# Optimization experiments

Measured on AMD Instinct MI355X. Metric: run time of the kernel, lower is better.

## Reference

```python
import jax, jax.numpy as jnp
import numpy as np

B = 64        # number of graph segments
BASE = 384    # mean verts per segment
LMAX = 512    # pad length (counts in [256, 512])
H_DIM = 256
H_DIV = 128   # h_dim // h_dim_div
HEADS = 4
DH = H_DIV // HEADS  # 32


def _counts(seed):
    rng = np.random.default_rng(seed)
    d = rng.integers(-128, 129, B)
    d[1::2] = -d[::2]            # paired so the total is exactly B*BASE
    return (BASE + d).astype(np.int64)


def _pad_indices(counts, L):
    # Gather indices/mask mapping packed ragged tokens -> padded [B, L].
    counts = np.asarray(counts)
    off = np.concatenate([[0], np.cumsum(counts)[:-1]])
    ar = np.arange(L)[None, :]
    mask = ar < counts[:, None]
    idx = np.where(mask, off[:, None] + ar, 0)
    return idx, mask


def setup_inputs() -> dict:
    key = jax.random.key(0)
    ks = jax.random.split(key, 16)
    src_num_verts = _counts(0)
    dst_num_verts = _counts(1)
    total = B * BASE  # 24576 for both src and dst

    def w(k, shape):
        return 0.02 * jax.random.normal(k, shape, jnp.float32)

    return {
        'src_h': jax.random.normal(ks[0], (total, H_DIM), jnp.float32),
        'dst_h': jax.random.normal(ks[1], (total, H_DIM), jnp.float32),
        'src_num_verts': src_num_verts,
        'dst_num_verts': dst_num_verts,
        # 1x1 Conv1d == linear over channels
        'Wq': w(ks[2], (H_DIV, H_DIM)), 'bq': w(ks[3], (H_DIV,)),
        'Wk': w(ks[4], (H_DIV, H_DIM)), 'bk': w(ks[5], (H_DIV,)),
        'Wv': w(ks[6], (H_DIV, H_DIM)), 'bv': w(ks[7], (H_DIV,)),
        'Wm': w(ks[8], (H_DIV, H_DIV)), 'bm': w(ks[9], (H_DIV,)),
        'W1': w(ks[10], (H_DIM, H_DIM + H_DIV)), 'b1': w(ks[11], (H_DIM,)),
        'g1': 1.0 + 0.1 * jax.random.normal(ks[12], (H_DIM,), jnp.float32),
        'be1': w(ks[13], (H_DIM,)),
        'rm1': w(ks[14], (H_DIM,)),
        'rv1': jax.random.uniform(ks[15], (H_DIM,), jnp.float32, 0.5, 1.5),
        'W2': w(jax.random.fold_in(key, 100), (H_DIM, H_DIM)),
        'b2': w(jax.random.fold_in(key, 101), (H_DIM,)),
        'g2': 1.0 + 0.1 * jax.random.normal(jax.random.fold_in(key, 102), (H_DIM,), jnp.float32),
        'be2': w(jax.random.fold_in(key, 103), (H_DIM,)),
        'rm2': w(jax.random.fold_in(key, 104), (H_DIM,)),
        'rv2': jax.random.uniform(jax.random.fold_in(key, 105), (H_DIM,), jnp.float32, 0.5, 1.5),
    }


def _bn(x, g, b, rm, rv):
    # BatchNorm1d in eval mode (running stats)
    return (x - rm) / jnp.sqrt(rv + 1e-5) * g + b


def reference(src_h, dst_h, src_num_verts, dst_num_verts,
              Wq, bq, Wk, bk, Wv, bv, Wm, bm,
              W1, b1, g1, be1, rm1, rv1,
              W2, b2, g2, be2, rm2, rv2):
    didx, dmask = _pad_indices(dst_num_verts, LMAX)
    sidx, smask = _pad_indices(src_num_verts, LMAX)

    # fused projections over all packed tokens (1x1 conv == matmul)
    q = src_h_proj = dst_h @ Wq.T + bq        # [Nd, H_DIV]
    k = src_h @ Wk.T + bk                     # [Ns, H_DIV]
    v = src_h @ Wv.T + bv

    # pad to block-diagonal batched form; channel c = d*HEADS + h per torch view
    qp = q[didx].reshape(B, LMAX, DH, HEADS)
    kp = k[sidx].reshape(B, LMAX, DH, HEADS)
    vp = v[sidx].reshape(B, LMAX, DH, HEADS)

    scores = jnp.einsum('bndh,bmdh->bhnm', qp, kp) / (DH ** 0.5)
    scores = jnp.where(jnp.asarray(smask)[:, None, None, :], scores, -1e9)
    attn = jax.nn.softmax(scores, axis=-1)
    msg = jnp.einsum('bhnm,bmdh->bndh', attn, vp).reshape(B, LMAX, H_DIV)
    msg = msg @ Wm.T + bm                     # merge conv

    bb, ii = np.nonzero(dmask)                # unpad back to packed layout
    h_msg = msg[bb, ii]                       # [Nd, H_DIV]

    x = jnp.concatenate([dst_h, h_msg], axis=-1)
    x = _bn(x @ W1.T + b1, g1, be1, rm1, rv1)
    x = jax.nn.relu(x)
    x = _bn(x @ W2.T + b2, g2, be2, rm2, rv2)
    return dst_h + x
```

## Files before the change

kernel.cpp:

```cpp
#include <hip/hip_runtime.h>
#include <hip/hip_bf16.h>
#include <math.h>

#define B_SEG 64
#define HDIM 256
#define HDIV 128
#define NHEADS 4
#define DH 32
#define VSTR 520
#define PSTR 136
#define QSC 0.17677669529663687f

typedef unsigned short u16;
typedef unsigned int u32;

typedef __attribute__((ext_vector_type(8))) short s8v;
typedef __attribute__((ext_vector_type(4))) float f4v;

__device__ __forceinline__ u16 f2bf(float f) {
    u32 v;
    __builtin_memcpy(&v, &f, 4);
    u32 r = v + 0x7fffu + ((v >> 16) & 1u);
    return (u16)(r >> 16);
}

__device__ __forceinline__ void async_cp16(const u16* g, u16* l) {
    __builtin_amdgcn_global_load_lds(
        (const __attribute__((address_space(1))) u32*)g,
        (__attribute__((address_space(3))) u32*)l, 16, 0, 0);
}

__global__ __launch_bounds__(256) void k_prep(
    const float* __restrict__ Wq, const float* __restrict__ bq,
    const float* __restrict__ Wk, const float* __restrict__ bk,
    const float* __restrict__ Wv, const float* __restrict__ bv,
    const float* __restrict__ Wm, const float* __restrict__ bm,
    const float* __restrict__ W1, const float* __restrict__ b1,
    const float* __restrict__ g1, const float* __restrict__ be1,
    const float* __restrict__ rm1, const float* __restrict__ rv1,
    const float* __restrict__ W2, const float* __restrict__ b2,
    const float* __restrict__ g2, const float* __restrict__ be2,
    const float* __restrict__ rm2, const float* __restrict__ rv2,
    const int* __restrict__ sc_raw, const int* __restrict__ dc_raw,
    const float* __restrict__ src_h, const float* __restrict__ dst_h,
    int* __restrict__ meta,
    u16* __restrict__ pWq, u16* __restrict__ pWkv,
    u16* __restrict__ pW1f, u16* __restrict__ pW2,
    float* __restrict__ bqp, float* __restrict__ bkvp,
    float* __restrict__ sc1, float* __restrict__ sh1,
    float* __restrict__ sc2, float* __restrict__ sh2,
    u16* __restrict__ srcb, u16* __restrict__ dstb, int ntot) {
    if (blockIdx.x < 1028) {
        int idx = blockIdx.x * 256 + threadIdx.x;
        if (idx < 32768) {
            int cp = idx >> 8, k = idx & 255;
            int c = ((cp & 31) << 2) | (cp >> 5);
            pWq[idx] = f2bf(Wq[c * 256 + k]);
        } else if (idx < 98304) {
            int i = idx - 32768;
            int rp = i >> 8, k = i & 255;
            int r = rp & 127;
            int c = ((r & 31) << 2) | (r >> 5);
            float v = (rp < 128) ? Wk[c * 256 + k] : Wv[c * 256 + k];
            pWkv[i] = f2bf(v);
        } else if (idx < 163840) {
            int i = idx - 98304;
            int o = i >> 8, k = i & 255;
            pW1f[o * 384 + k] = f2bf(W1[o * 384 + k]);
        } else if (idx < 196608) {
            int i = idx - 163840;
            int o = i >> 7, cp = i & 127;
            int c = ((cp & 31) << 2) | (cp >> 5);
            float acc = 0.f;
            for (int j = 0; j < 128; j++)
                acc += W1[o * 384 + 256 + j] * Wm[j * 128 + c];
            pW1f[o * 384 + 256 + cp] = f2bf(acc);
        } else if (idx < 262144) {
            int i = idx - 196608;
            pW2[i] = f2bf(W2[i]);
        } else if (idx < 263168) {
            int p = idx - 262144;
            if (p < 128) {
                int c = ((p & 31) << 2) | (p >> 5);
                bqp[p] = bq[c] * QSC;
            } else if (p < 384) {
                int r = p - 128; int rr = r & 127;
                int c = ((rr & 31) << 2) | (rr >> 5);
                bkvp[r] = (r < 128) ? bk[c] : bv[c];
            } else if (p < 640) {
                int o = p - 384;
                float bsum = 0.f;
                for (int j = 0; j < 128; j++)
                    bsum += W1[o * 384 + 256 + j] * bm[j];
                float s = g1[o] * rsqrtf(rv1[o] + 1e-5f);
                sc1[o] = s;
                sh1[o] = (b1[o] + bsum - rm1[o]) * s + be1[o];
            } else if (p < 896) {
                int o = p - 640;
                float s = g2[o] * rsqrtf(rv2[o] + 1e-5f);
                sc2[o] = s;
                sh2[o] = (b2[o] - rm2[o]) * s + be2[o];
            }
        }
    } else if (blockIdx.x == 1028) {
        if (threadIdx.x == 0) {
            bool is64 = (sc_raw[1] == 0);
            int so = 0, dofs = 0;
            for (int i = 0; i < B_SEG; i++) {
                int s = is64 ? sc_raw[2 * i] : sc_raw[i];
                int d = is64 ? dc_raw[2 * i] : dc_raw[i];
                meta[i] = s; meta[64 + i] = d;
                meta[128 + i] = so; meta[192 + i] = dofs;
                so += s; dofs += d;
            }
        }
    } else {
        int i = (blockIdx.x - 1029) * 256 + threadIdx.x;
        int half = ntot * 64;
        const float4* s;
        u16* o;
        int j = i;
        if (i < half) { s = (const float4*)src_h; o = srcb; }
        else { s = (const float4*)dst_h; o = dstb; j = i - half; }
        float4 v = s[j];
        ushort4 u = {f2bf(v.x), f2bf(v.y), f2bf(v.z), f2bf(v.w)};
        ((ushort4*)o)[j] = u;
    }
}

__device__ __forceinline__ void gemm_body(
    const u16* __restrict__ A, int lda,
    const u16* __restrict__ A2, int lda2, int K1,
    const u16* __restrict__ Bw, int K, int m0, int n0,
    const float* __restrict__ scale, const float* __restrict__ shift,
    const float* __restrict__ resid,
    void* __restrict__ Cout, int ldc, int flags,
    u16* Al, u16* Bl) {
    int tid = threadIdx.x;
    int w = tid >> 6, lane = tid & 63;
    int wm = w & 1, wn = w >> 1;
    int l15 = lane & 15, quad = lane >> 4;
    int srow = w * 32 + (lane >> 3);
    int scol = (lane & 7) << 3;
    f4v acc[4][4] = {};

    for (int k0 = 0; k0 < K; k0 += 64) {
        const u16* Ag; int aL, acol;
        if (k0 < K1) { Ag = A; aL = lda; acol = k0; }
        else { Ag = A2; aL = lda2; acol = k0 - K1; }
#pragma unroll
        for (int j = 0; j < 4; j++) {
            async_cp16(&Ag[(size_t)(m0 + srow + j * 8) * aL + acol + scol],
                       Al + w * 2048 + j * 512);
            async_cp16(&Bw[(size_t)(n0 + srow + j * 8) * K + k0 + scol],
                       Bl + w * 2048 + j * 512);
        }
        __syncthreads();
#pragma unroll
        for (int kk = 0; kk < 2; kk++) {
            s8v af[4], bf[4];
#pragma unroll
            for (int i = 0; i < 4; i++)
                af[i] = *(const s8v*)(&Al[(wm * 64 + i * 16 + l15) * 64
                                          + kk * 32 + quad * 8]);
#pragma unroll
            for (int j = 0; j < 4; j++)
                bf[j] = *(const s8v*)(&Bl[(wn * 64 + j * 16 + l15) * 64
                                          + kk * 32 + quad * 8]);
#pragma unroll
            for (int i = 0; i < 4; i++)
#pragma unroll
                for (int j = 0; j < 4; j++)
                    acc[i][j] = __builtin_amdgcn_mfma_f32_16x16x32_bf16(
                        af[i], bf[j], acc[i][j], 0, 0, 0);
        }
        __syncthreads();
    }
#pragma unroll
    for (int i = 0; i < 4; i++) {
#pragma unroll
        for (int j = 0; j < 4; j++) {
            int n = n0 + wn * 64 + j * 16 + l15;
            float sc = scale ? scale[n] : 1.f;
            float sh = shift ? shift[n] : 0.f;
#pragma unroll
            for (int r = 0; r < 4; r++) {
                int m = m0 + wm * 64 + i * 16 + quad * 4 + r;
                float v = acc[i][j][r];
                if (flags & 4) v *= QSC;
                v = v * sc + sh;
                if (flags & 1) v = fmaxf(v, 0.f);
                if (resid) v += resid[(size_t)m * 256 + n];
                if (flags & 2) ((float*)Cout)[(size_t)m * ldc + n] = v;
                else ((u16*)Cout)[(size_t)m * ldc + n] = f2bf(v);
            }
        }
    }
}

__global__ __launch_bounds__(256) void k_qkv(
    const u16* __restrict__ dstb, const u16* __restrict__ srcb,
    const u16* __restrict__ pWq, const u16* __restrict__ pWkv,
    const float* __restrict__ bqp, const float* __restrict__ bkvp,
    u16* __restrict__ qb, u16* __restrict__ kvb) {
    __shared__ u16 Al[8192];
    __shared__ u16 Bl[8192];
    int m0 = blockIdx.x * 128;
    if (blockIdx.y == 0)
        gemm_body(dstb, 256, dstb, 256, 256, pWq, 256, m0, 0,
                  nullptr, bqp, nullptr, qb, 128, 4, Al, Bl);
    else
        gemm_body(srcb, 256, srcb, 256, 256, pWkv, 256, m0, (blockIdx.y - 1) * 128,
                  nullptr, bkvp, nullptr, kvb, 256, 0, Al, Bl);
}

__global__ __launch_bounds__(256) void k_gemm(
    const u16* __restrict__ A, int lda,
    const u16* __restrict__ A2, int lda2, int K1,
    const u16* __restrict__ Bw, int K,
    const float* __restrict__ scale, const float* __restrict__ shift,
    const float* __restrict__ resid,
    void* __restrict__ Cout, int ldc, int flags) {
    __shared__ u16 Al[8192];
    __shared__ u16 Bl[8192];
    gemm_body(A, lda, A2, lda2, K1, Bw, K, blockIdx.x * 128, blockIdx.y * 128,
              scale, shift, resid, Cout, ldc, flags, Al, Bl);
}

__global__ __launch_bounds__(512, 4) void k_attn(
    const u16* __restrict__ qb, const u16* __restrict__ kvb,
    const int* __restrict__ meta, u16* __restrict__ msgb) {
    extern __shared__ u16 sm[];
    u16* Vl = sm;
    u16* Pl = sm + 32 * VSTR;
    int b = blockIdx.x, h = blockIdx.y, z = blockIdx.z;
    int ns = meta[b], nd = meta[64 + b];
    int soff = meta[128 + b], doff = meta[192 + b];
    int tid = threadIdx.x, w = tid >> 6, lane = tid & 63;
    int l15 = lane & 15, quad = lane >> 4;

    {
        int m = tid;
        if (m < ns) {
            uint4 vv[4];
            const uint4* vs =
                (const uint4*)&kvb[(size_t)(soff + m) * 256 + 128 + h * 32];
#pragma unroll
            for (int q4 = 0; q4 < 4; q4++) vv[q4] = vs[q4];
            const u16* pv = (const u16*)vv;
#pragma unroll
            for (int d = 0; d < 32; d++) Vl[d * VSTR + m] = pv[d];
        } else {
#pragma unroll
            for (int d = 0; d < 32; d++) Vl[d * VSTR + m] = 0;
        }
    }
    __syncthreads();

    int nc = (ns + 127) >> 7;
    u16* Pw = Pl + w * 16 * PSTR;
    const u16* kb = kvb + h * 32;

    for (int s0 = (z * 8 + w) * 16; s0 < nd; s0 += 256) {
        int qr = min(s0 + l15, nd - 1);
        s8v aq = *(const s8v*)&qb[(size_t)(doff + qr) * 128 + h * 32 + quad * 8];

        float lsum[4] = {0.f, 0.f, 0.f, 0.f};
        f4v oa0 = {0.f, 0.f, 0.f, 0.f}, oa1 = {0.f, 0.f, 0.f, 0.f};
#pragma unroll
        for (int c = 0; c < 4; c++) {
            if (c < nc) {
                f4v e[8];
#pragma unroll
                for (int tt = 0; tt < 8; tt++) {
                    int kr = min(c * 128 + tt * 16 + l15, ns - 1);
                    s8v bk = *(const s8v*)&kb[(size_t)(soff + kr) * 256 + quad * 8];
                    e[tt] = __builtin_amdgcn_mfma_f32_16x16x32_bf16(
                        aq, bk, (f4v){0.f, 0.f, 0.f, 0.f}, 0, 0, 0);
                }
#pragma unroll
                for (int tt = 0; tt < 8; tt++) {
                    bool ok = (c * 128 + tt * 16 + l15) < ns;
#pragma unroll
                    for (int r = 0; r < 4; r++) {
                        float ev = ok ? __expf(e[tt][r]) : 0.f;
                        e[tt][r] = ev;
                        lsum[r] += ev;
                    }
                }
#pragma unroll
                for (int tt = 0; tt < 8; tt++)
#pragma unroll
                    for (int r = 0; r < 4; r++)
                        Pw[(quad * 4 + r) * PSTR + tt * 16 + l15] =
                            f2bf(e[tt][r]);
#pragma unroll
                for (int kc = 0; kc < 4; kc++) {
                    s8v ap = *(const s8v*)&Pw[l15 * PSTR + kc * 32 + quad * 8];
                    s8v bv0 = *(const s8v*)&Vl[l15 * VSTR + c * 128 + kc * 32 + quad * 8];
                    s8v bv1 = *(const s8v*)&Vl[(16 + l15) * VSTR + c * 128 + kc * 32 + quad * 8];
                    oa0 = __builtin_amdgcn_mfma_f32_16x16x32_bf16(ap, bv0, oa0, 0, 0, 0);
                    oa1 = __builtin_amdgcn_mfma_f32_16x16x32_bf16(ap, bv1, oa1, 0, 0, 0);
                }
            }
        }
        float inv[4];
#pragma unroll
        for (int r = 0; r < 4; r++) {
            float s_ = lsum[r];
#pragma unroll
            for (int x = 1; x < 16; x <<= 1) s_ += __shfl_xor(s_, x, 16);
            inv[r] = 1.f / s_;
        }
#pragma unroll
        for (int r = 0; r < 4; r++) {
            int row = s0 + quad * 4 + r;
            if (row < nd) {
                size_t base = (size_t)(doff + row) * 128 + h * 32;
                msgb[base + l15] = f2bf(oa0[r] * inv[r]);
                msgb[base + 16 + l15] = f2bf(oa1[r] * inv[r]);
            }
        }
    }
}

extern "C" void kernel_launch(void* const* d_in, const int* in_sizes, int n_in,
                              void* d_out, int out_size, void* d_ws, size_t ws_size,
                              hipStream_t stream) {
    const float* src_h = (const float*)d_in[0];
    const float* dst_h = (const float*)d_in[1];
    const int* snv = (const int*)d_in[2];
    const int* dnv = (const int*)d_in[3];
    const float* Wq = (const float*)d_in[4];  const float* bq = (const float*)d_in[5];
    const float* Wk = (const float*)d_in[6];  const float* bk = (const float*)d_in[7];
    const float* Wv = (const float*)d_in[8];  const float* bv = (const float*)d_in[9];
    const float* Wm = (const float*)d_in[10]; const float* bm = (const float*)d_in[11];
    const float* W1 = (const float*)d_in[12]; const float* b1 = (const float*)d_in[13];
    const float* g1 = (const float*)d_in[14]; const float* be1 = (const float*)d_in[15];
    const float* rm1 = (const float*)d_in[16]; const float* rv1 = (const float*)d_in[17];
    const float* W2 = (const float*)d_in[18]; const float* b2 = (const float*)d_in[19];
    const float* g2 = (const float*)d_in[20]; const float* be2 = (const float*)d_in[21];
    const float* rm2 = (const float*)d_in[22]; const float* rv2 = (const float*)d_in[23];

    int ntot = out_size / HDIM;
    int mt = ntot / 128;

    char* ws = (char*)d_ws;
    int* meta = (int*)ws;
    float* bqp = (float*)(ws + 4096);
    float* bkvp = (float*)(ws + 4608);
    float* sc1 = (float*)(ws + 6144);
    float* sh1 = (float*)(ws + 7168);
    float* sc2 = (float*)(ws + 8192);
    float* sh2 = (float*)(ws + 9216);
    u16* pWq = (u16*)(ws + 16384);
    u16* pWkv = (u16*)(ws + 81920);
    u16* pW1f = (u16*)(ws + 212992);
    u16* pW2 = (u16*)(ws + 409600);
    u16* srcb = (u16*)(ws + 1048576);
    u16* x1b = srcb;
    u16* dstb = (u16*)(ws + 13631488);

    u16* qb = (u16*)d_out;
    u16* kvb = qb + (size_t)ntot * 128;
    u16* msgb = kvb + (size_t)ntot * 256;

    hipFuncSetAttribute((const void*)k_attn,
                        hipFuncAttributeMaxDynamicSharedMemorySize, 131072);

    k_prep<<<dim3(1029 + ntot / 2), dim3(256), 0, stream>>>(
        Wq, bq, Wk, bk, Wv, bv, Wm, bm, W1, b1, g1, be1, rm1, rv1,
        W2, b2, g2, be2, rm2, rv2, snv, dnv, src_h, dst_h, meta,
        pWq, pWkv, pW1f, pW2, bqp, bkvp, sc1, sh1, sc2, sh2,
        srcb, dstb, ntot);
    k_qkv<<<dim3(mt, 3), dim3(256), 0, stream>>>(
        dstb, srcb, pWq, pWkv, bqp, bkvp, qb, kvb);
    k_attn<<<dim3(B_SEG, NHEADS, 2), dim3(512), 68096, stream>>>(
        qb, kvb, meta, msgb);
    k_gemm<<<dim3(mt, 2), dim3(256), 0, stream>>>(
        dstb, 256, msgb, 128, 256, pW1f, 384, sc1, sh1, nullptr, x1b, 256, 1);
    k_gemm<<<dim3(mt, 2), dim3(256), 0, stream>>>(
        x1b, 256, x1b, 256, 256, pW2, 256, sc2, sh2, dst_h, d_out, 256, 2);
}
```

Measured before the change: 238.9 us.

## Compute transposed attention scores to keep P in registers, dropping LDS staging

The attention kernel now computes S^T (keys as the MFMA A operand, queries as B), so each lane's exp'd score fragment already matches the B-operand layout of the P·V MFMA. The P tile no longer round-trips through shared memory. V is stored in LDS with a permuted column order so its A-operand reads line up with that register layout. LDS drops to a static V buffer only, which lowers the shared-memory footprint and removes per-tile LDS writes and reads. Row sums and output stores are reorganised to suit the transposed layout, and outputs are now written as vectorised 4-element stores.

```diff
diff --git a/kernel.cpp b/kernel.cpp
--- a/kernel.cpp
+++ b/kernel.cpp
@@ -7,8 +7,7 @@
 #define HDIV 128
 #define NHEADS 4
 #define DH 32
-#define VSTR 520
-#define PSTR 136
+#define VTSTR 520
 #define QSC 0.17677669529663687f
 
 typedef unsigned short u16;
@@ -230,9 +229,7 @@
 __global__ __launch_bounds__(512, 4) void k_attn(
     const u16* __restrict__ qb, const u16* __restrict__ kvb,
     const int* __restrict__ meta, u16* __restrict__ msgb) {
-    extern __shared__ u16 sm[];
-    u16* Vl = sm;
-    u16* Pl = sm + 32 * VSTR;
+    __shared__ u16 Vl[32 * VTSTR];
     int b = blockIdx.x, h = blockIdx.y, z = blockIdx.z;
     int ns = meta[b], nd = meta[64 + b];
     int soff = meta[128 + b], doff = meta[192 + b];
@@ -241,6 +238,7 @@
 
     {
         int m = tid;
+        int col = (m & ~31) | ((m & 0xC) << 1) | ((m & 16) >> 2) | (m & 3);
         if (m < ns) {
             uint4 vv[4];
             const uint4* vs =
@@ -249,77 +247,71 @@
             for (int q4 = 0; q4 < 4; q4++) vv[q4] = vs[q4];
             const u16* pv = (const u16*)vv;
 #pragma unroll
-            for (int d = 0; d < 32; d++) Vl[d * VSTR + m] = pv[d];
+            for (int d = 0; d < 32; d++) Vl[d * VTSTR + col] = pv[d];
         } else {
 #pragma unroll
-            for (int d = 0; d < 32; d++) Vl[d * VSTR + m] = 0;
+            for (int d = 0; d < 32; d++) Vl[d * VTSTR + col] = 0;
         }
     }
     __syncthreads();
 
-    int nc = (ns + 127) >> 7;
-    u16* Pw = Pl + w * 16 * PSTR;
-    const u16* kb = kvb + h * 32;
+    const u16* kbase = kvb + (size_t)soff * 256 + h * 32;
 
     for (int s0 = (z * 8 + w) * 16; s0 < nd; s0 += 256) {
         int qr = min(s0 + l15, nd - 1);
         s8v aq = *(const s8v*)&qb[(size_t)(doff + qr) * 128 + h * 32 + quad * 8];
 
-        float lsum[4] = {0.f, 0.f, 0.f, 0.f};
+        float lsum = 0.f;
         f4v oa0 = {0.f, 0.f, 0.f, 0.f}, oa1 = {0.f, 0.f, 0.f, 0.f};
 #pragma unroll
         for (int c = 0; c < 4; c++) {
-            if (c < nc) {
+            if (c * 128 < ns) {
                 f4v e[8];
 #pragma unroll
                 for (int tt = 0; tt < 8; tt++) {
                     int kr = min(c * 128 + tt * 16 + l15, ns - 1);
-                    s8v bk = *(const s8v*)&kb[(size_t)(soff + kr) * 256 + quad * 8];
+                    s8v ak = *(const s8v*)&kbase[(size_t)kr * 256 + quad * 8];
                     e[tt] = __builtin_amdgcn_mfma_f32_16x16x32_bf16(
-                        aq, bk, (f4v){0.f, 0.f, 0.f, 0.f}, 0, 0, 0);
+                        ak, aq, (f4v){0.f, 0.f, 0.f, 0.f}, 0, 0, 0);
                 }
 #pragma unroll
                 for (int tt = 0; tt < 8; tt++) {
-                    bool ok = (c * 128 + tt * 16 + l15) < ns;
 #pragma unroll
                     for (int r = 0; r < 4; r++) {
-                        float ev = ok ? __expf(e[tt][r]) : 0.f;
+                        int key = c * 128 + tt * 16 + quad * 4 + r;
+                        float ev = (key < ns) ? __expf(e[tt][r]) : 0.f;
                         e[tt][r] = ev;
-                        lsum[r] += ev;
+                        lsum += ev;
                     }
                 }
 #pragma unroll
-                for (int tt = 0; tt < 8; tt++)
-#pragma unroll
-                    for (int r = 0; r < 4; r++)
-                        Pw[(quad * 4 + r) * PSTR + tt * 16 + l15] =
-                            f2bf(e[tt][r]);
-#pragma unroll
-                for (int kc = 0; kc < 4; kc++) {
-                    s8v ap = *(const s8v*)&Pw[l15 * PSTR + kc * 32 + quad * 8];
-                    s8v bv0 = *(const s8v*)&Vl[l15 * VSTR + c * 128 + kc * 32 + quad * 8];
-                    s8v bv1 = *(const s8v*)&Vl[(16 + l15) * VSTR + c * 128 + kc * 32 + quad * 8];
-                    oa0 = __builtin_amdgcn_mfma_f32_16x16x32_bf16(ap, bv0, oa0, 0, 0, 0);
-                    oa1 = __builtin_amdgcn_mfma_f32_16x16x32_bf16(ap, bv1, oa1, 0, 0, 0);
+                for (int g = 0; g < 4; g++) {
+                    s8v pb;
+                    u16* pbp = (u16*)&pb;
+#pragma unroll
+                    for (int j = 0; j < 4; j++) pbp[j] = f2bf(e[2 * g][j]);
+#pragma unroll
+                    for (int j = 0; j < 4; j++) pbp[4 + j] = f2bf(e[2 * g + 1][j]);
+                    int colb = c * 128 + g * 32 + quad * 8;
+                    s8v av0 = *(const s8v*)&Vl[(size_t)l15 * VTSTR + colb];
+                    s8v av1 = *(const s8v*)&Vl[(size_t)(16 + l15) * VTSTR + colb];
+                    oa0 = __builtin_amdgcn_mfma_f32_16x16x32_bf16(av0, pb, oa0, 0, 0, 0);
+                    oa1 = __builtin_amdgcn_mfma_f32_16x16x32_bf16(av1, pb, oa1, 0, 0, 0);
                 }
             }
         }
-        float inv[4];
-#pragma unroll
-        for (int r = 0; r < 4; r++) {
-            float s_ = lsum[r];
-#pragma unroll
-            for (int x = 1; x < 16; x <<= 1) s_ += __shfl_xor(s_, x, 16);
-            inv[r] = 1.f / s_;
-        }
-#pragma unroll
-        for (int r = 0; r < 4; r++) {
-            int row = s0 + quad * 4 + r;
-            if (row < nd) {
-                size_t base = (size_t)(doff + row) * 128 + h * 32;
-                msgb[base + l15] = f2bf(oa0[r] * inv[r]);
-                msgb[base + 16 + l15] = f2bf(oa1[r] * inv[r]);
-            }
+        lsum += __shfl_xor(lsum, 16, 64);
+        lsum += __shfl_xor(lsum, 32, 64);
+        float inv = 1.f / lsum;
+        int row = s0 + l15;
+        if (row < nd) {
+            size_t base = (size_t)(doff + row) * 128 + h * 32;
+            ushort4 o0 = {f2bf(oa0[0] * inv), f2bf(oa0[1] * inv),
+                          f2bf(oa0[2] * inv), f2bf(oa0[3] * inv)};
+            ushort4 o1 = {f2bf(oa1[0] * inv), f2bf(oa1[1] * inv),
+                          f2bf(oa1[2] * inv), f2bf(oa1[3] * inv)};
+            *(ushort4*)&msgb[base + quad * 4] = o0;
+            *(ushort4*)&msgb[base + 16 + quad * 4] = o1;
         }
     }
 }
@@ -365,9 +357,6 @@
     u16* kvb = qb + (size_t)ntot * 128;
     u16* msgb = kvb + (size_t)ntot * 256;
 
-    hipFuncSetAttribute((const void*)k_attn,
-                        hipFuncAttributeMaxDynamicSharedMemorySize, 131072);
-
     k_prep<<<dim3(1029 + ntot / 2), dim3(256), 0, stream>>>(
         Wq, bq, Wk, bk, Wv, bv, Wm, bm, W1, b1, g1, be1, rm1, rv1,
         W2, b2, g2, be2, rm2, rv2, snv, dnv, src_h, dst_h, meta,
@@ -375,7 +364,7 @@
         srcb, dstb, ntot);
     k_qkv<<<dim3(mt, 3), dim3(256), 0, stream>>>(
         dstb, srcb, pWq, pWkv, bqp, bkvp, qb, kvb);
-    k_attn<<<dim3(B_SEG, NHEADS, 2), dim3(512), 68096, stream>>>(
+    k_attn<<<dim3(B_SEG, NHEADS, 2), dim3(512), 0, stream>>>(
         qb, kvb, meta, msgb);
     k_gemm<<<dim3(mt, 2), dim3(256), 0, stream>>>(
         dstb, 256, msgb, 128, 256, pW1f, 384, sc1, sh1, nullptr, x1b, 256, 1);
```

After: 244.5 us. +2.4%, slower.
